# Optimization experiments

Hardware: AMD Instinct MI355X
Metric: run time of the kernel (lower is better)

## Reference

```python
import jax, jax.numpy as jnp
import numpy as np

WINDOW = (2, 7, 7)
DIM = 128
HEADS = 4
N = WINDOW[0] * WINDOW[1] * WINDOW[2]  # 98
TABLE = (2 * WINDOW[0] - 1) * (2 * WINDOW[1] - 1) * (2 * WINDOW[2] - 1)  # 507


def _rel_pos_index():
    d, h, w = WINDOW
    coords = np.stack(np.meshgrid(np.arange(d), np.arange(h), np.arange(w), indexing='ij'))  # [3,d,h,w]
    cf = coords.reshape(3, -1)  # [3, N]
    rel = cf[:, :, None] - cf[:, None, :]  # [3, N, N]
    rel = rel.transpose(1, 2, 0).copy()
    rel[:, :, 0] += d - 1
    rel[:, :, 1] += h - 1
    rel[:, :, 2] += w - 1
    rel[:, :, 0] *= (2 * h - 1) * (2 * w - 1)
    rel[:, :, 1] *= 2 * w - 1
    return jnp.asarray(rel.sum(-1), dtype=jnp.int32)  # [N, N]

REL_IDX = _rel_pos_index()


def setup_inputs() -> dict:
    key = jax.random.key(0)
    ks = jax.random.split(key, 8)
    B_, nW = 2048, 64
    x = jax.random.normal(ks[0], (B_, N, DIM), dtype=jnp.float32)
    mask = jax.random.normal(ks[1], (nW, N, N), dtype=jnp.float32)
    qkv_w = jax.random.normal(ks[2], (3 * DIM, DIM), dtype=jnp.float32) * (DIM ** -0.5)
    qkv_b = jnp.zeros((3 * DIM,), dtype=jnp.float32)
    rpb_table = jax.random.normal(ks[3], (TABLE, HEADS), dtype=jnp.float32) * 0.02
    proj_w = jax.random.normal(ks[4], (DIM, DIM), dtype=jnp.float32) * (DIM ** -0.5)
    proj_b = jnp.zeros((DIM,), dtype=jnp.float32)
    return {"x": x, "mask": mask, "qkv_w": qkv_w, "qkv_b": qkv_b,
            "rpb_table": rpb_table, "proj_w": proj_w, "proj_b": proj_b}


def reference(x, mask, qkv_w, qkv_b, rpb_table, proj_w, proj_b):
    B_, n, C = x.shape
    hd = C // HEADS
    scale = hd ** -0.5
    qkv = x @ qkv_w.T + qkv_b  # [B_, N, 3C]
    qkv = qkv.reshape(B_, n, 3, HEADS, hd).transpose(2, 0, 3, 1, 4)  # [3, B_, H, N, hd]
    q, k, v = qkv[0], qkv[1], qkv[2]
    attn = jnp.einsum('bhnd,bhmd->bhnm', q * scale, k)  # [B_, H, N, N]
    bias = rpb_table[REL_IDX.reshape(-1)].reshape(n, n, HEADS)  # gather
    attn = attn + bias.transpose(2, 0, 1)[None]  # [B_, H, N, N]
    nW = mask.shape[0]
    attn = attn.reshape(B_ // nW, nW, HEADS, n, n) + mask[None, :, None]
    attn = jax.nn.softmax(attn.reshape(B_, HEADS, n, n), axis=-1)
    out = jnp.einsum('bhnm,bhmd->bhnd', attn, v)  # [B_, H, N, hd]
    out = out.transpose(0, 2, 1, 3).reshape(B_, n, C)
    return out @ proj_w.T + proj_b
```

## Files before the change

kernel.cpp:

```cpp
#include <hip/hip_runtime.h>
#include <hip/hip_bf16.h>

#define NTOK 98
#define CDIM 128
#define SCALE 0.17677669529663687f
#define LOG2E 1.4426950408889634f
#define NEG_BIG -1e30f
#define CMBW 112

typedef short bf16x8 __attribute__((ext_vector_type(8)));
typedef short bf16x4 __attribute__((ext_vector_type(4)));
typedef float f32x4 __attribute__((ext_vector_type(4)));

#define MFMA32(a,b,c) __builtin_amdgcn_mfma_f32_16x16x32_bf16(a,b,c,0,0,0)

#if __has_builtin(__builtin_amdgcn_mfma_f32_16x16x16_bf16)
#define MFMA16(a,b,c) __builtin_amdgcn_mfma_f32_16x16x16_bf16(a,b,c,0,0,0)
#elif __has_builtin(__builtin_amdgcn_mfma_f32_16x16x16bf16_1k)
#define MFMA16(a,b,c) __builtin_amdgcn_mfma_f32_16x16x16bf16_1k(a,b,c,0,0,0)
#else
__device__ __forceinline__ f32x4 mfma16_asm(bf16x4 a, bf16x4 b, f32x4 c) {
  asm("v_mfma_f32_16x16x16_bf16 %0, %1, %2, %0" : "+v"(c) : "v"(a), "v"(b));
  return c;
}
#define MFMA16(a,b,c) mfma16_asm(a,b,c)
#endif

#if __has_builtin(__builtin_amdgcn_exp2f)
#define EXP2F(x) __builtin_amdgcn_exp2f(x)
#else
#define EXP2F(x) exp2f(x)
#endif
#if __has_builtin(__builtin_amdgcn_rcpf)
#define RCPF(x) __builtin_amdgcn_rcpf(x)
#else
#define RCPF(x) (1.f / (x))
#endif

__device__ __forceinline__ unsigned short f2bf(float f) {
  __hip_bfloat16 h = __float2bfloat16(f);
  unsigned short u;
  __builtin_memcpy(&u, &h, 2);
  return u;
}
__device__ __forceinline__ float bf2f(unsigned short b) {
  union { unsigned u; float f; } v; v.u = ((unsigned)b) << 16; return v.f;
}
__device__ __forceinline__ bf16x4 cvt4(f32x4 v) {
  __hip_bfloat162 a = __float22bfloat162_rn(make_float2(v[0], v[1]));
  __hip_bfloat162 b = __float22bfloat162_rn(make_float2(v[2], v[3]));
  bf16x4 r;
  __builtin_memcpy(&r, &a, 4);
  __builtin_memcpy(((char*)&r) + 4, &b, 4);
  return r;
}

__device__ __forceinline__ int swzK(int row, int col) {
  return row * 128 + (col ^ ((row & 7) << 3));
}

__device__ __forceinline__ bf16x8 ldfrag(const float* __restrict__ p) {
  float4 a = *(const float4*)p;
  float4 b = *(const float4*)(p + 4);
  bf16x8 fr;
  fr[0]=(short)f2bf(a.x); fr[1]=(short)f2bf(a.y); fr[2]=(short)f2bf(a.z); fr[3]=(short)f2bf(a.w);
  fr[4]=(short)f2bf(b.x); fr[5]=(short)f2bf(b.y); fr[6]=(short)f2bf(b.z); fr[7]=(short)f2bf(b.w);
  return fr;
}

__device__ __forceinline__ int pcode(int t) {
  int d = t / 49, r = t % 49;
  return d * 169 + (r / 7) * 13 + (r % 7);
}

__global__ __launch_bounds__(512)
void prep_w(const float* __restrict__ qkv_w, const float* __restrict__ qkv_b,
            const float* __restrict__ proj_w, const float* __restrict__ proj_b,
            unsigned short* __restrict__ qpre, unsigned short* __restrict__ ppre,
            float* __restrict__ bpre)
{
  int gid = blockIdx.x * 512 + threadIdx.x;
  if (gid < 6144) {
    int t = gid >> 8, rem = gid & 255, kk = rem >> 6, ln = rem & 63;
    int row = t * 16 + (ln & 15), col = kk * 32 + (ln >> 4) * 8;
    float sc = (row < CDIM) ? SCALE * LOG2E : 1.f;
    const float* s = qkv_w + (size_t)row * CDIM + col;
    unsigned short* d = qpre + (size_t)gid * 8;
#pragma unroll
    for (int e = 0; e < 8; ++e) d[e] = f2bf(s[e] * sc);
  } else if (gid < 8192) {
    int f2 = gid - 6144;
    int t = f2 >> 8, rem = f2 & 255, kk = rem >> 6, ln = rem & 63;
    const float* s = proj_w + (size_t)(t * 16 + (ln & 15)) * CDIM + kk * 32 + (ln >> 4) * 8;
    unsigned short* d = ppre + (size_t)f2 * 8;
#pragma unroll
    for (int e = 0; e < 8; ++e) d[e] = f2bf(s[e]);
  } else {
    int i = gid - 8192;
    if (i < 384) bpre[i] = qkv_b[i] * (i < CDIM ? SCALE * LOG2E : 1.f);
    else if (i < 512) bpre[i] = proj_b[i - 384];
  }
}

__global__ __launch_bounds__(256)
void prep_cmb(const float* __restrict__ mask, const float* __restrict__ rpb,
              float* __restrict__ cmb, int nW)
{
  const int total = 256 * NTOK * CMBW;
  for (int idx = blockIdx.x * 256 + threadIdx.x; idx < total; idx += gridDim.x * 256) {
    int row = idx / CMBW, n = idx - row * CMBW;
    int wh = row / NTOK, m = row - wh * NTOK;
    int w = wh >> 2, h = wh & 3;
    float v = NEG_BIG;
    if (n < NTOK)
      v = (mask[((size_t)w * NTOK + m) * NTOK + n]
           + rpb[(pcode(m) - pcode(n) + 253) * 4 + h]) * LOG2E;
    cmb[idx] = v;
  }
}

template<bool PRE>
__global__ __launch_bounds__(512, 4)
void win_attn(const float* __restrict__ x, const float* __restrict__ mask,
              const float* __restrict__ qkv_w, const float* __restrict__ qkv_b,
              const float* __restrict__ rpb, const float* __restrict__ proj_w,
              const float* __restrict__ proj_b, float* __restrict__ out, int nW,
              const float* __restrict__ cmb, const unsigned short* __restrict__ qpre,
              const unsigned short* __restrict__ ppre, const float* __restrict__ bpre)
{
  __shared__ __align__(16) unsigned short xs[(PRE ? 112 : 98) * 128];
  __shared__ __align__(16) unsigned short kbuf[98 * 128];
  __shared__ __align__(16) unsigned short vbuf[128 * 100];
  __shared__ unsigned short rpbL[PRE ? 2 : 2028];
  __shared__ short mcode[PRE ? 2 : 112];

  const int tid = threadIdx.x;
  const int lane = tid & 63;
  const int wv = tid >> 6;
  const int lm = lane & 15;
  const int lg = lane >> 4;
  const int blk = blockIdx.x;
  const int wmod = blk % nW;
  const float* __restrict__ xblk = x + (size_t)blk * (NTOK * CDIM);
  const float* __restrict__ maskw = mask + (size_t)wmod * (NTOK * NTOK);

  if constexpr (!PRE) {
    if (tid < 112) mcode[tid] = (short)(tid < NTOK ? pcode(tid) : 0);
    for (int i = tid; i < 2028; i += 512) rpbL[i] = f2bf(rpb[i]);
  }
  for (int v = tid; v < NTOK * 32; v += 512) {
    int row = v >> 5, c4 = (v & 31) << 2;
    float4 f = *(const float4*)(xblk + row * CDIM + c4);
    f32x4 fv; fv[0]=f.x; fv[1]=f.y; fv[2]=f.z; fv[3]=f.w;
    bf16x4 pk = cvt4(fv);
    *(bf16x4*)&xs[swzK(row, c4)] = pk;
  }
  __syncthreads();

  auto wq = [&](int t, int kk) -> bf16x8 {
    if constexpr (PRE) return *(const bf16x8*)&qpre[(size_t)((t * 4 + kk) * 64 + lane) * 8];
    else return ldfrag(qkv_w + (size_t)(t * 16 + lm) * CDIM + kk * 32 + lg * 8);
  };

  {
    bf16x8 Bk[4], Bv[4];
#pragma unroll
    for (int kk = 0; kk < 4; ++kk) { Bk[kk] = wq(8 + wv, kk); Bv[kk] = wq(16 + wv, kk); }
    const float4 bk4 = *(const float4*)((PRE ? bpre : qkv_b) + CDIM + wv * 16 + lg * 4);
    const float  bv_ = (PRE ? bpre : qkv_b)[2 * CDIM + wv * 16 + lm];
    for (int mi = 0; mi < 7; ++mi) {
      int arow = mi * 16 + lm; if (arow > 97) arow = 97;
      bf16x8 A[4];
#pragma unroll
      for (int kk = 0; kk < 4; ++kk) A[kk] = *(const bf16x8*)&xs[swzK(arow, kk * 32 + lg * 8)];
      f32x4 ak = {0.f,0.f,0.f,0.f}, av = {0.f,0.f,0.f,0.f};
#pragma unroll
      for (int kk = 0; kk < 4; ++kk) {
        ak = MFMA32(Bk[kk], A[kk], ak);
        av = MFMA32(A[kk], Bv[kk], av);
      }
      int ktok = mi * 16 + lm;
      if (ktok < NTOK) {
        f32x4 t;
#pragma unroll
        for (int r = 0; r < 4; ++r) t[r] = ak[r] + ((const float*)&bk4)[r];
        *(bf16x4*)&kbuf[swzK(ktok, wv * 16 + lg * 4)] = cvt4(t);
      }
      int vtok0 = mi * 16 + lg * 4;
      if (vtok0 < 100) {
        f32x4 t;
#pragma unroll
        for (int r = 0; r < 4; ++r) t[r] = av[r] + bv_;
        *(bf16x4*)&vbuf[(size_t)(wv * 16 + lm) * 100 + vtok0] = cvt4(t);
      }
    }
  }

  const bool have1 = (wv < 6);
  const int hh0 = wv / 7, mi0 = wv % 7;
  const int mi1 = wv + 1;

  bf16x4 bq[2][2][2];
#pragma unroll
  for (int j = 0; j < 2; ++j) {
    if (j == 0 || have1) {
      const int mi = j ? mi1 : mi0, hh = j ? 1 : hh0;
      int arow = mi * 16 + lm; if (arow > 97) arow = 97;
      bf16x8 Xf[4];
#pragma unroll
      for (int kk = 0; kk < 4; ++kk) Xf[kk] = *(const bf16x8*)&xs[swzK(arow, kk * 32 + lg * 8)];
#pragma unroll
      for (int g = 0; g < 2; ++g) {
        const int h = 2 * g + hh;
#pragma unroll
        for (int ct = 0; ct < 2; ++ct) {
          const int t = h * 2 + ct;
          f32x4 acc = {0.f,0.f,0.f,0.f};
#pragma unroll
          for (int kk = 0; kk < 4; ++kk) acc = MFMA32(wq(t, kk), Xf[kk], acc);
          const float4 qb4 = *(const float4*)((PRE ? bpre : qkv_b) + t * 16 + lg * 4);
          f32x4 tq;
#pragma unroll
          for (int r = 0; r < 4; ++r) {
            float vq = acc[r] + ((const float*)&qb4)[r];
            if constexpr (!PRE) vq *= SCALE * LOG2E;
            tq[r] = vq;
          }
          bq[j][g][ct] = cvt4(tq);
        }
      }
    }
  }
  __syncthreads();

#pragma unroll
  for (int g = 0; g < 2; ++g) {
#pragma unroll
    for (int j = 0; j < 2; ++j) {
      if (j == 0 || have1) {
        const int mi = j ? mi1 : mi0, hh = j ? 1 : hh0;
        const int h = 2 * g + hh, cb = h * 32;
        f32x4 s[7];
        __builtin_amdgcn_s_setprio(1);
#pragma unroll
        for (int nj = 0; nj < 7; ++nj) {
          int krow = nj * 16 + lm; if (krow > 97) krow = 97;
          bf16x4 k0 = *(const bf16x4*)&kbuf[swzK(krow, cb + lg * 4)];
          bf16x4 k1 = *(const bf16x4*)&kbuf[swzK(krow, cb + 16 + lg * 4)];
          f32x4 z = {0.f,0.f,0.f,0.f};
          z = MFMA16(k0, bq[j][g][0], z);
          s[nj] = MFMA16(k1, bq[j][g][1], z);
        }
        __builtin_amdgcn_s_setprio(0);
        const int m = mi * 16 + lm;
        const int mclamp = m > 97 ? 97 : m;
        float sum = 0.f;
        if constexpr (PRE) {
          const float* __restrict__ cp =
              cmb + ((size_t)(wmod * 4 + h) * NTOK + mclamp) * CMBW + lg * 4;
#pragma unroll
          for (int nj = 0; nj < 7; ++nj) {
            float4 cv = *(const float4*)(cp + nj * 16);
#pragma unroll
            for (int r = 0; r < 4; ++r) {
              float e = EXP2F(s[nj][r] + ((const float*)&cv)[r]);
              s[nj][r] = e; sum += e;
            }
          }
        } else {
          const int cm4 = ((int)mcode[mclamp]) * 4 + h + 1012;
          const float* __restrict__ mrow = maskw + mclamp * NTOK;
#pragma unroll
          for (int nj = 0; nj < 7; ++nj) {
            const int n0 = nj * 16 + lg * 4;
#pragma unroll
            for (int r = 0; r < 4; ++r) {
              int n = n0 + r;
              float val = NEG_BIG;
              if (n < NTOK)
                val = s[nj][r] + (mrow[n] + bf2f(rpbL[cm4 - ((int)mcode[n]) * 4])) * LOG2E;
              float e = EXP2F(val);
              s[nj][r] = e; sum += e;
            }
          }
        }
        sum += __shfl_xor(sum, 16);
        sum += __shfl_xor(sum, 32);
        const float inv = RCPF(sum);
        float invr[4];
#pragma unroll
        for (int r = 0; r < 4; ++r) invr[r] = __shfl(inv, lg * 4 + r);
        bf16x4 pp[7];
#pragma unroll
        for (int nj = 0; nj < 7; ++nj) pp[nj] = cvt4(s[nj]);
#pragma unroll
        for (int dt = 0; dt < 2; ++dt) {
          const int d = cb + dt * 16 + lm;
          f32x4 acc = {0.f,0.f,0.f,0.f};
          __builtin_amdgcn_s_setprio(1);
#pragma unroll
          for (int nj = 0; nj < 7; ++nj) {
            const int vc = nj < 6 ? nj * 16 + lg * 4 : 96;
            bf16x4 bv = *(const bf16x4*)&vbuf[(size_t)d * 100 + vc];
            acc = MFMA16(pp[nj], bv, acc);
          }
          __builtin_amdgcn_s_setprio(0);
#pragma unroll
          for (int r = 0; r < 4; ++r) {
            int m2 = mi * 16 + lg * 4 + r;
            if (PRE || m2 < NTOK) xs[swzK(m2, d)] = f2bf(acc[r] * invr[r]);
          }
        }
      }
    }
  }
  __syncthreads();

  {
    bf16x8 Bp[4];
#pragma unroll
    for (int kk = 0; kk < 4; ++kk) {
      if constexpr (PRE) Bp[kk] = *(const bf16x8*)&ppre[(size_t)((wv * 4 + kk) * 64 + lane) * 8];
      else Bp[kk] = ldfrag(proj_w + (size_t)(wv * 16 + lm) * CDIM + kk * 32 + lg * 8);
    }
    const float4 pb4 = *(const float4*)((PRE ? bpre + 384 : proj_b) + wv * 16 + lg * 4);
    float* __restrict__ outb = out + (size_t)blk * (NTOK * CDIM);
    for (int mi = 0; mi < 7; ++mi) {
      int orow = mi * 16 + lm;
      if (!PRE && orow > 97) orow = 97;
      f32x4 acc = {0.f,0.f,0.f,0.f};
#pragma unroll
      for (int kk = 0; kk < 4; ++kk) {
        bf16x8 Bo = *(const bf16x8*)&xs[swzK(orow, kk * 32 + lg * 8)];
        acc = MFMA32(Bp[kk], Bo, acc);
      }
      int tok = mi * 16 + lm;
      if (tok < NTOK) {
        float4 o4;
        o4.x = acc[0] + pb4.x; o4.y = acc[1] + pb4.y;
        o4.z = acc[2] + pb4.z; o4.w = acc[3] + pb4.w;
        *(float4*)(outb + (size_t)tok * CDIM + wv * 16 + lg * 4) = o4;
      }
    }
  }
}

extern "C" void kernel_launch(void* const* d_in, const int* in_sizes, int n_in,
                              void* d_out, int out_size, void* d_ws, size_t ws_size,
                              hipStream_t stream) {
  const float* x      = (const float*)d_in[0];
  const float* mask   = (const float*)d_in[1];
  const float* qkv_w  = (const float*)d_in[2];
  const float* qkv_b  = (const float*)d_in[3];
  const float* rpb    = (const float*)d_in[4];
  const float* proj_w = (const float*)d_in[5];
  const float* proj_b = (const float*)d_in[6];
  int B  = in_sizes[0] / (NTOK * CDIM);
  int nW = in_sizes[1] / (NTOK * NTOK);

  const size_t CMB_B  = (size_t)256 * NTOK * CMBW * 4;
  const size_t QPRE_B = 24 * 4 * 64 * 8 * 2;
  const size_t PPRE_B = 8 * 4 * 64 * 8 * 2;
  const size_t BIAS_B = 512 * 4;
  const size_t need = CMB_B + QPRE_B + PPRE_B + BIAS_B;

  if (ws_size >= need) {
    float* cmb = (float*)d_ws;
    unsigned short* qpre = (unsigned short*)((char*)d_ws + CMB_B);
    unsigned short* ppre = (unsigned short*)((char*)d_ws + CMB_B + QPRE_B);
    float* bpre = (float*)((char*)d_ws + CMB_B + QPRE_B + PPRE_B);
    hipLaunchKernelGGL(prep_w, dim3(17), dim3(512), 0, stream,
                       qkv_w, qkv_b, proj_w, proj_b, qpre, ppre, bpre);
    hipLaunchKernelGGL(prep_cmb, dim3(1024), dim3(256), 0, stream, mask, rpb, cmb, nW);
    hipLaunchKernelGGL(win_attn<true>, dim3(B), dim3(512), 0, stream,
                       x, mask, qkv_w, qkv_b, rpb, proj_w, proj_b, (float*)d_out, nW,
                       cmb, qpre, ppre, bpre);
  } else {
    hipLaunchKernelGGL(win_attn<false>, dim3(B), dim3(512), 0, stream,
                       x, mask, qkv_w, qkv_b, rpb, proj_w, proj_b, (float*)d_out, nW,
                       (const float*)nullptr, (const unsigned short*)nullptr,
                       (const unsigned short*)nullptr, (const float*)nullptr);
  }
}
```

Before: 138.2 us.

## Split K/V staging into two head groups to halve LDS and raise occupancy

K and V are now projected and staged in two passes of 64 channels (two heads each), so the kbuf and vbuf shared buffers are half the size and xs no longer needs padding rows. Launch bounds go from 4 to 6 blocks per SM to use the freed LDS. Attention for the first head group is computed and held in registers, then the second group's K/V is staged with extra barriers before the outputs are written back to xs. In exchange the kernel gains two more __syncthreads and splits the K/V projection across wave halves, and the higher block target may push register pressure into spills.

New measurement: 172.2 us. +24.6%, slower.

```diff
diff --git a/kernel.cpp b/kernel.cpp
--- a/kernel.cpp
+++ b/kernel.cpp
@@ -57,6 +57,9 @@
 
 __device__ __forceinline__ int swzK(int row, int col) {
   return row * 128 + (col ^ ((row & 7) << 3));
+}
+__device__ __forceinline__ int swz64(int row, int col) {
+  return row * 64 + (col ^ ((row & 7) << 3));
 }
 
 __device__ __forceinline__ bf16x8 ldfrag(const float* __restrict__ p) {
@@ -120,7 +123,7 @@
 }
 
 template<bool PRE>
-__global__ __launch_bounds__(512, 4)
+__global__ __launch_bounds__(512, 6)
 void win_attn(const float* __restrict__ x, const float* __restrict__ mask,
               const float* __restrict__ qkv_w, const float* __restrict__ qkv_b,
               const float* __restrict__ rpb, const float* __restrict__ proj_w,
@@ -128,9 +131,9 @@
               const float* __restrict__ cmb, const unsigned short* __restrict__ qpre,
               const unsigned short* __restrict__ ppre, const float* __restrict__ bpre)
 {
-  __shared__ __align__(16) unsigned short xs[(PRE ? 112 : 98) * 128];
-  __shared__ __align__(16) unsigned short kbuf[98 * 128];
-  __shared__ __align__(16) unsigned short vbuf[128 * 100];
+  __shared__ __align__(16) unsigned short xs[98 * 128];
+  __shared__ __align__(16) unsigned short kbuf[98 * 64];
+  __shared__ __align__(16) unsigned short vbuf[64 * 100];
   __shared__ unsigned short rpbL[PRE ? 2 : 2028];
   __shared__ short mcode[PRE ? 2 : 112];
 
@@ -143,6 +146,7 @@
   const int wmod = blk % nW;
   const float* __restrict__ xblk = x + (size_t)blk * (NTOK * CDIM);
   const float* __restrict__ maskw = mask + (size_t)wmod * (NTOK * NTOK);
+  const float* __restrict__ bias = PRE ? bpre : qkv_b;
 
   if constexpr (!PRE) {
     if (tid < 112) mcode[tid] = (short)(tid < NTOK ? pcode(tid) : 0);
@@ -152,8 +156,7 @@
     int row = v >> 5, c4 = (v & 31) << 2;
     float4 f = *(const float4*)(xblk + row * CDIM + c4);
     f32x4 fv; fv[0]=f.x; fv[1]=f.y; fv[2]=f.z; fv[3]=f.w;
-    bf16x4 pk = cvt4(fv);
-    *(bf16x4*)&xs[swzK(row, c4)] = pk;
+    *(bf16x4*)&xs[swzK(row, c4)] = cvt4(fv);
   }
   __syncthreads();
 
@@ -162,44 +165,57 @@
     else return ldfrag(qkv_w + (size_t)(t * 16 + lm) * CDIM + kk * 32 + lg * 8);
   };
 
-  {
-    bf16x8 Bk[4], Bv[4];
-#pragma unroll
-    for (int kk = 0; kk < 4; ++kk) { Bk[kk] = wq(8 + wv, kk); Bv[kk] = wq(16 + wv, kk); }
-    const float4 bk4 = *(const float4*)((PRE ? bpre : qkv_b) + CDIM + wv * 16 + lg * 4);
-    const float  bv_ = (PRE ? bpre : qkv_b)[2 * CDIM + wv * 16 + lm];
-    for (int mi = 0; mi < 7; ++mi) {
-      int arow = mi * 16 + lm; if (arow > 97) arow = 97;
-      bf16x8 A[4];
-#pragma unroll
-      for (int kk = 0; kk < 4; ++kk) A[kk] = *(const bf16x8*)&xs[swzK(arow, kk * 32 + lg * 8)];
-      f32x4 ak = {0.f,0.f,0.f,0.f}, av = {0.f,0.f,0.f,0.f};
-#pragma unroll
-      for (int kk = 0; kk < 4; ++kk) {
-        ak = MFMA32(Bk[kk], A[kk], ak);
-        av = MFMA32(A[kk], Bv[kk], av);
-      }
-      int ktok = mi * 16 + lm;
-      if (ktok < NTOK) {
-        f32x4 t;
-#pragma unroll
-        for (int r = 0; r < 4; ++r) t[r] = ak[r] + ((const float*)&bk4)[r];
-        *(bf16x4*)&kbuf[swzK(ktok, wv * 16 + lg * 4)] = cvt4(t);
-      }
-      int vtok0 = mi * 16 + lg * 4;
-      if (vtok0 < 100) {
-        f32x4 t;
-#pragma unroll
-        for (int r = 0; r < 4; ++r) t[r] = av[r] + bv_;
-        *(bf16x4*)&vbuf[(size_t)(wv * 16 + lm) * 100 + vtok0] = cvt4(t);
-      }
-    }
-  }
+  auto stage_kv = [&](int g) {
+    if (wv < 4) {
+      bf16x8 Bk[4];
+#pragma unroll
+      for (int kk = 0; kk < 4; ++kk) Bk[kk] = wq(8 + g * 4 + wv, kk);
+      const float4 bk4 = *(const float4*)(bias + CDIM + g * 64 + wv * 16 + lg * 4);
+      for (int mi = 0; mi < 7; ++mi) {
+        int arow = mi * 16 + lm; if (arow > 97) arow = 97;
+        bf16x8 A[4];
+#pragma unroll
+        for (int kk = 0; kk < 4; ++kk) A[kk] = *(const bf16x8*)&xs[swzK(arow, kk * 32 + lg * 8)];
+        f32x4 ak = {0.f,0.f,0.f,0.f};
+#pragma unroll
+        for (int kk = 0; kk < 4; ++kk) ak = MFMA32(Bk[kk], A[kk], ak);
+        int ktok = mi * 16 + lm;
+        if (ktok < NTOK) {
+          f32x4 t;
+#pragma unroll
+          for (int r = 0; r < 4; ++r) t[r] = ak[r] + ((const float*)&bk4)[r];
+          *(bf16x4*)&kbuf[swz64(ktok, wv * 16 + lg * 4)] = cvt4(t);
+        }
+      }
+    } else {
+      bf16x8 Bv[4];
+#pragma unroll
+      for (int kk = 0; kk < 4; ++kk) Bv[kk] = wq(16 + g * 4 + (wv - 4), kk);
+      const float bv_ = bias[2 * CDIM + g * 64 + (wv - 4) * 16 + lm];
+      for (int mi = 0; mi < 7; ++mi) {
+        int arow = mi * 16 + lm; if (arow > 97) arow = 97;
+        bf16x8 A[4];
+#pragma unroll
+        for (int kk = 0; kk < 4; ++kk) A[kk] = *(const bf16x8*)&xs[swzK(arow, kk * 32 + lg * 8)];
+        f32x4 av = {0.f,0.f,0.f,0.f};
+#pragma unroll
+        for (int kk = 0; kk < 4; ++kk) av = MFMA32(A[kk], Bv[kk], av);
+        int vtok0 = mi * 16 + lg * 4;
+        if (vtok0 < 100) {
+          f32x4 t;
+#pragma unroll
+          for (int r = 0; r < 4; ++r) t[r] = av[r] + bv_;
+          *(bf16x4*)&vbuf[(size_t)((wv - 4) * 16 + lm) * 100 + vtok0] = cvt4(t);
+        }
+      }
+    }
+  };
 
   const bool have1 = (wv < 6);
   const int hh0 = wv / 7, mi0 = wv % 7;
   const int mi1 = wv + 1;
 
+  stage_kv(0);
   bf16x4 bq[2][2][2];
 #pragma unroll
   for (int j = 0; j < 2; ++j) {
@@ -218,7 +234,7 @@
           f32x4 acc = {0.f,0.f,0.f,0.f};
 #pragma unroll
           for (int kk = 0; kk < 4; ++kk) acc = MFMA32(wq(t, kk), Xf[kk], acc);
-          const float4 qb4 = *(const float4*)((PRE ? bpre : qkv_b) + t * 16 + lg * 4);
+          const float4 qb4 = *(const float4*)(bias + t * 16 + lg * 4);
           f32x4 tq;
 #pragma unroll
           for (int r = 0; r < 4; ++r) {
@@ -233,85 +249,111 @@
   }
   __syncthreads();
 
-#pragma unroll
-  for (int g = 0; g < 2; ++g) {
-#pragma unroll
-    for (int j = 0; j < 2; ++j) {
-      if (j == 0 || have1) {
-        const int mi = j ? mi1 : mi0, hh = j ? 1 : hh0;
-        const int h = 2 * g + hh, cb = h * 32;
-        f32x4 s[7];
-        __builtin_amdgcn_s_setprio(1);
-#pragma unroll
-        for (int nj = 0; nj < 7; ++nj) {
-          int krow = nj * 16 + lm; if (krow > 97) krow = 97;
-          bf16x4 k0 = *(const bf16x4*)&kbuf[swzK(krow, cb + lg * 4)];
-          bf16x4 k1 = *(const bf16x4*)&kbuf[swzK(krow, cb + 16 + lg * 4)];
-          f32x4 z = {0.f,0.f,0.f,0.f};
-          z = MFMA16(k0, bq[j][g][0], z);
-          s[nj] = MFMA16(k1, bq[j][g][1], z);
+  auto attn_unit = [&](int j, int g, bf16x4* og) {
+    const int mi = j ? mi1 : mi0, hh = j ? 1 : hh0;
+    const int h = 2 * g + hh, cbl = hh * 32;
+    f32x4 s[7];
+    __builtin_amdgcn_s_setprio(1);
+#pragma unroll
+    for (int nj = 0; nj < 7; ++nj) {
+      int krow = nj * 16 + lm; if (krow > 97) krow = 97;
+      bf16x4 k0 = *(const bf16x4*)&kbuf[swz64(krow, cbl + lg * 4)];
+      bf16x4 k1 = *(const bf16x4*)&kbuf[swz64(krow, cbl + 16 + lg * 4)];
+      f32x4 z = {0.f,0.f,0.f,0.f};
+      z = MFMA16(k0, bq[j][g][0], z);
+      s[nj] = MFMA16(k1, bq[j][g][1], z);
+    }
+    __builtin_amdgcn_s_setprio(0);
+    const int m = mi * 16 + lm;
+    const int mclamp = m > 97 ? 97 : m;
+    float sum = 0.f;
+    if constexpr (PRE) {
+      const float* __restrict__ cp =
+          cmb + ((size_t)(wmod * 4 + h) * NTOK + mclamp) * CMBW + lg * 4;
+#pragma unroll
+      for (int nj = 0; nj < 7; ++nj) {
+        float4 cv = *(const float4*)(cp + nj * 16);
+#pragma unroll
+        for (int r = 0; r < 4; ++r) {
+          float e = EXP2F(s[nj][r] + ((const float*)&cv)[r]);
+          s[nj][r] = e; sum += e;
         }
-        __builtin_amdgcn_s_setprio(0);
-        const int m = mi * 16 + lm;
-        const int mclamp = m > 97 ? 97 : m;
-        float sum = 0.f;
-        if constexpr (PRE) {
-          const float* __restrict__ cp =
-              cmb + ((size_t)(wmod * 4 + h) * NTOK + mclamp) * CMBW + lg * 4;
-#pragma unroll
-          for (int nj = 0; nj < 7; ++nj) {
-            float4 cv = *(const float4*)(cp + nj * 16);
-#pragma unroll
-            for (int r = 0; r < 4; ++r) {
-              float e = EXP2F(s[nj][r] + ((const float*)&cv)[r]);
-              s[nj][r] = e; sum += e;
-            }
-          }
-        } else {
-          const int cm4 = ((int)mcode[mclamp]) * 4 + h + 1012;
-          const float* __restrict__ mrow = maskw + mclamp * NTOK;
-#pragma unroll
-          for (int nj = 0; nj < 7; ++nj) {
-            const int n0 = nj * 16 + lg * 4;
-#pragma unroll
-            for (int r = 0; r < 4; ++r) {
-              int n = n0 + r;
-              float val = NEG_BIG;
-              if (n < NTOK)
-                val = s[nj][r] + (mrow[n] + bf2f(rpbL[cm4 - ((int)mcode[n]) * 4])) * LOG2E;
-              float e = EXP2F(val);
-              s[nj][r] = e; sum += e;
-            }
-          }
+      }
+    } else {
+      const int cm4 = ((int)mcode[mclamp]) * 4 + h + 1012;
+      const float* __restrict__ mrow = maskw + mclamp * NTOK;
+#pragma unroll
+      for (int nj = 0; nj < 7; ++nj) {
+        const int n0 = nj * 16 + lg * 4;
+#pragma unroll
+        for (int r = 0; r < 4; ++r) {
+          int n = n0 + r;
+          float val = NEG_BIG;
+          if (n < NTOK)
+            val = s[nj][r] + (mrow[n] + bf2f(rpbL[cm4 - ((int)mcode[n]) * 4])) * LOG2E;
+          float e = EXP2F(val);
+          s[nj][r] = e; sum += e;
         }
-        sum += __shfl_xor(sum, 16);
-        sum += __shfl_xor(sum, 32);
-        const float inv = RCPF(sum);
-        float invr[4];
-#pragma unroll
-        for (int r = 0; r < 4; ++r) invr[r] = __shfl(inv, lg * 4 + r);
-        bf16x4 pp[7];
-#pragma unroll
-        for (int nj = 0; nj < 7; ++nj) pp[nj] = cvt4(s[nj]);
-#pragma unroll
-        for (int dt = 0; dt < 2; ++dt) {
-          const int d = cb + dt * 16 + lm;
-          f32x4 acc = {0.f,0.f,0.f,0.f};
-          __builtin_amdgcn_s_setprio(1);
-#pragma unroll
-          for (int nj = 0; nj < 7; ++nj) {
-            const int vc = nj < 6 ? nj * 16 + lg * 4 : 96;
-            bf16x4 bv = *(const bf16x4*)&vbuf[(size_t)d * 100 + vc];
-            acc = MFMA16(pp[nj], bv, acc);
-          }
-          __builtin_amdgcn_s_setprio(0);
-#pragma unroll
-          for (int r = 0; r < 4; ++r) {
-            int m2 = mi * 16 + lg * 4 + r;
-            if (PRE || m2 < NTOK) xs[swzK(m2, d)] = f2bf(acc[r] * invr[r]);
-          }
-        }
-      }
+      }
+    }
+    sum += __shfl_xor(sum, 16);
+    sum += __shfl_xor(sum, 32);
+    const float inv = RCPF(sum);
+    float invr[4];
+#pragma unroll
+    for (int r = 0; r < 4; ++r) invr[r] = __shfl(inv, lg * 4 + r);
+    bf16x4 pp[7];
+#pragma unroll
+    for (int nj = 0; nj < 7; ++nj) pp[nj] = cvt4(s[nj]);
+#pragma unroll
+    for (int dt = 0; dt < 2; ++dt) {
+      const int dl = cbl + dt * 16 + lm;
+      f32x4 acc = {0.f,0.f,0.f,0.f};
+      __builtin_amdgcn_s_setprio(1);
+#pragma unroll
+      for (int nj = 0; nj < 7; ++nj) {
+        const int vc = nj < 6 ? nj * 16 + lg * 4 : 96;
+        bf16x4 bv = *(const bf16x4*)&vbuf[(size_t)dl * 100 + vc];
+        acc = MFMA16(pp[nj], bv, acc);
+      }
+      __builtin_amdgcn_s_setprio(0);
+      f32x4 t;
+#pragma unroll
+      for (int r = 0; r < 4; ++r) t[r] = acc[r] * invr[r];
+      og[dt] = cvt4(t);
+    }
+  };
+
+  auto write_o = [&](int j, int g, const bf16x4* og) {
+    const int mi = j ? mi1 : mi0, hh = j ? 1 : hh0;
+#pragma unroll
+    for (int dt = 0; dt < 2; ++dt) {
+      const int d = (2 * g + hh) * 32 + dt * 16 + lm;
+#pragma unroll
+      for (int r = 0; r < 4; ++r) {
+        int m2 = mi * 16 + lg * 4 + r;
+        if (m2 < NTOK) xs[swzK(m2, d)] = (unsigned short)og[dt][r];
+      }
+    }
+  };
+
+  bf16x4 og0[2], og1[2];
+  attn_unit(0, 0, og0);
+  if (have1) attn_unit(1, 0, og1);
+  __syncthreads();
+
+  stage_kv(1);
+  __syncthreads();
+
+  write_o(0, 0, og0);
+  if (have1) write_o(1, 0, og1);
+  {
+    bf16x4 ot[2];
+    attn_unit(0, 1, ot);
+    write_o(0, 1, ot);
+    if (have1) {
+      attn_unit(1, 1, ot);
+      write_o(1, 1, ot);
     }
   }
   __syncthreads();
@@ -326,8 +368,7 @@
     const float4 pb4 = *(const float4*)((PRE ? bpre + 384 : proj_b) + wv * 16 + lg * 4);
     float* __restrict__ outb = out + (size_t)blk * (NTOK * CDIM);
     for (int mi = 0; mi < 7; ++mi) {
-      int orow = mi * 16 + lm;
-      if (!PRE && orow > 97) orow = 97;
+      int orow = mi * 16 + lm; if (orow > 97) orow = 97;
       f32x4 acc = {0.f,0.f,0.f,0.f};
 #pragma unroll
       for (int kk = 0; kk < 4; ++kk) {
```
